# Performance work log

Measured on AMD Instinct MI355X. Metric: run time of the kernel, lower is better.

## Reference

```python
import jax, jax.numpy as jnp
import numpy as np

B, D, E, T, H = 16384, 1024, 8, 4, 512


def setup_inputs() -> dict:
    key = jax.random.key(0)
    ks = jax.random.split(key, 7)
    s_e = 1.0 / np.sqrt(D)
    s_t = 1.0 / np.sqrt(H)
    return {
        "x": jax.random.normal(ks[0], (B, D), dtype=jnp.float32),
        "We": jax.random.uniform(ks[1], (E, D, H), minval=-s_e, maxval=s_e, dtype=jnp.float32),
        "be": jax.random.uniform(ks[2], (E, H), minval=-s_e, maxval=s_e, dtype=jnp.float32),
        "Wg": jax.random.uniform(ks[3], (T, D, E), minval=-s_e, maxval=s_e, dtype=jnp.float32),
        "bg": jax.random.uniform(ks[4], (T, E), minval=-s_e, maxval=s_e, dtype=jnp.float32),
        "Wt": jax.random.uniform(ks[5], (T, H, 1), minval=-s_t, maxval=s_t, dtype=jnp.float32),
        "bt": jax.random.uniform(ks[6], (T, 1), minval=-s_t, maxval=s_t, dtype=jnp.float32),
    }


def reference(x, We, be, Wg, bg, Wt, bt):
    # Experts: [B, E, H] -- batched GEMM over all experts at once
    expert_out = jnp.einsum("bd,edh->beh", x, We) + be[None, :, :]
    # Gates per task: logits [B, T, E], softmax over experts
    gate_logits = jnp.einsum("bd,tde->bte", x, Wg) + bg[None, :, :]
    gate_w = jax.nn.softmax(gate_logits, axis=-1)
    # Weighted sum of expert outputs per task: [B, T, H]
    mixed = jnp.einsum("bte,beh->bth", gate_w, expert_out)
    # Task heads: [B, T, 1]
    task_out = jnp.einsum("bth,tho->bto", mixed, Wt) + bt[None, :, :]
    # Match original: list of T tensors [B, 1] -> stacked [T, B, 1]
    return jnp.transpose(task_out, (1, 0, 2))
```

## Files before the change

### kernel.cpp

```cpp
#include <hip/hip_runtime.h>
#include <math.h>


typedef float  f32x4  __attribute__((ext_vector_type(4)));
typedef short  bf16x8 __attribute__((ext_vector_type(8)));

#define WFRAG_OFF_BYTES 262272

__device__ __forceinline__ void cvt_pair(float f0, float f1, unsigned int& hi, unsigned int& lo) {
  unsigned int u0 = __float_as_uint(f0), u1 = __float_as_uint(f1);
  unsigned int r0 = u0 + 0x7FFFu + ((u0 >> 16) & 1u);
  unsigned int r1 = u1 + 0x7FFFu + ((u1 >> 16) & 1u);
  float h0 = __uint_as_float(r0 & 0xFFFF0000u);
  float h1 = __uint_as_float(r1 & 0xFFFF0000u);
  hi = (r0 >> 16) | (r1 & 0xFFFF0000u);
  float l0 = f0 - h0, l1 = f1 - h1;
  unsigned int s0 = __float_as_uint(l0), s1 = __float_as_uint(l1);
  unsigned int q0 = s0 + 0x7FFFu + ((s0 >> 16) & 1u);
  unsigned int q1 = s1 + 0x7FFFu + ((s1 >> 16) & 1u);
  lo = (q0 >> 16) | (q1 & 0xFFFF0000u);
}

__global__ __launch_bounds__(256) void mmoe_precompute(
    const float* __restrict__ We, const float* __restrict__ be,
    const float* __restrict__ Wg, const float* __restrict__ Wt,
    float* __restrict__ ws)
{
  float* Wcomb = ws;
  float* cbias = ws + 65536;
  const int tid = threadIdx.x, lane = tid & 63, w = tid >> 6;
  const int pairid = blockIdx.x * 4 + w;
  const int e = pairid >> 10, d = pairid & 1023;

  const float* werow = We + (size_t)pairid * 512;
  float a0 = 0.f, a1 = 0.f, a2 = 0.f, a3 = 0.f;
#pragma unroll
  for (int j = 0; j < 8; ++j) {
    int h = lane + j * 64;
    float wv = werow[h];
    a0 = fmaf(wv, Wt[h],        a0);
    a1 = fmaf(wv, Wt[512 + h],  a1);
    a2 = fmaf(wv, Wt[1024 + h], a2);
    a3 = fmaf(wv, Wt[1536 + h], a3);
  }
#pragma unroll
  for (int m = 1; m < 64; m <<= 1) {
    a0 += __shfl_xor(a0, m, 64); a1 += __shfl_xor(a1, m, 64);
    a2 += __shfl_xor(a2, m, 64); a3 += __shfl_xor(a3, m, 64);
  }
  if (lane == 0) {
    Wcomb[d * 64 + 32 + 0 * 8 + e] = a0;
    Wcomb[d * 64 + 32 + 1 * 8 + e] = a1;
    Wcomb[d * 64 + 32 + 2 * 8 + e] = a2;
    Wcomb[d * 64 + 32 + 3 * 8 + e] = a3;
  }
  if (e == 0 && lane < 32) {
    int t = lane >> 3, ee = lane & 7;
    Wcomb[d * 64 + t * 8 + ee] = Wg[t * 8192 + d * 8 + ee];
  }
  if (d == 0) {
    float b0 = 0.f, b1 = 0.f, b2 = 0.f, b3 = 0.f;
#pragma unroll
    for (int j = 0; j < 8; ++j) {
      int h = lane + j * 64;
      float bv = be[e * 512 + h];
      b0 = fmaf(bv, Wt[h],        b0);
      b1 = fmaf(bv, Wt[512 + h],  b1);
      b2 = fmaf(bv, Wt[1024 + h], b2);
      b3 = fmaf(bv, Wt[1536 + h], b3);
    }
#pragma unroll
    for (int m = 1; m < 64; m <<= 1) {
      b0 += __shfl_xor(b0, m, 64); b1 += __shfl_xor(b1, m, 64);
      b2 += __shfl_xor(b2, m, 64); b3 += __shfl_xor(b3, m, 64);
    }
    if (lane == 0) {
      cbias[0 * 8 + e] = b0; cbias[1 * 8 + e] = b1;
      cbias[2 * 8 + e] = b2; cbias[3 * 8 + e] = b3;
    }
  }
}

__global__ __launch_bounds__(256) void mmoe_swizzle(const float* __restrict__ Wc,
                                                    uint4* __restrict__ wf)
{
  const int idx = blockIdx.x * 256 + threadIdx.x;
  const int ks = idx >> 9;
  const int rem = idx & 511;
  const int vn = rem >> 6, l = rem & 63;
  const int v = vn >> 2, nf = vn & 3;
  const int n = nf * 16 + (l & 15);
  const int kbase = ks * 32 + (l >> 4) * 8;
  unsigned int pk[4];
#pragma unroll
  for (int p = 0; p < 4; ++p) {
    float f0 = Wc[(size_t)(kbase + 2 * p) * 64 + n];
    float f1 = Wc[(size_t)(kbase + 2 * p + 1) * 64 + n];
    unsigned int hi, lo;
    cvt_pair(f0, f1, hi, lo);
    pk[p] = v ? lo : hi;
  }
  uint4 val; val.x = pk[0]; val.y = pk[1]; val.z = pk[2]; val.w = pk[3];
  wf[idx] = val;
}

__global__ __launch_bounds__(64, 1) void mmoe_main(
    const float* __restrict__ x,
    const float* __restrict__ bgp,
    const float* __restrict__ btp,
    const float* __restrict__ ws,
    float* __restrict__ out)
{
  __shared__ float cmat[1024];
  const int l  = threadIdx.x;
  const int b0g = blockIdx.x * 16;
  const float* cbias = ws + 65536;
  const bf16x8* __restrict__ bptr =
      (const bf16x8*)((const unsigned char*)ws + WFRAG_OFF_BYTES);

  const float4* __restrict__ xptr =
      (const float4*)(x + (size_t)(b0g + (l & 15)) * 1024) + (l >> 4) * 2;

  float4 xbuf[4][2];
  bf16x8 breg[2][8];
  f32x4  acc[4];
#pragma unroll
  for (int nf = 0; nf < 4; ++nf) acc[nf] = (f32x4){0.f, 0.f, 0.f, 0.f};

#pragma unroll
  for (int p = 0; p < 4; ++p) { xbuf[p][0] = xptr[p * 8]; xbuf[p][1] = xptr[p * 8 + 1]; }
#pragma unroll
  for (int vn = 0; vn < 8; ++vn) breg[0][vn] = bptr[vn * 64 + l];
#pragma unroll
  for (int vn = 0; vn < 8; ++vn) breg[1][vn] = bptr[512 + vn * 64 + l];

  union UC { unsigned int u[4]; bf16x8 v; };

#define STEP(S)                                                                      \
  {                                                                                  \
    float4 xa = xbuf[(S) & 3][0], xb = xbuf[(S) & 3][1];                             \
    if ((S) + 4 < 32) {                                                              \
      xbuf[(S) & 3][0] = xptr[((S) + 4) * 8];                                        \
      xbuf[(S) & 3][1] = xptr[((S) + 4) * 8 + 1];                                    \
    }                                                                                \
    UC Ah, Al;                                                                       \
    cvt_pair(xa.x, xa.y, Ah.u[0], Al.u[0]);                                          \
    cvt_pair(xa.z, xa.w, Ah.u[1], Al.u[1]);                                          \
    cvt_pair(xb.x, xb.y, Ah.u[2], Al.u[2]);                                          \
    cvt_pair(xb.z, xb.w, Ah.u[3], Al.u[3]);                                          \
    acc[0] = __builtin_amdgcn_mfma_f32_16x16x32_bf16(Ah.v, breg[(S) & 1][0], acc[0], 0, 0, 0); \
    acc[1] = __builtin_amdgcn_mfma_f32_16x16x32_bf16(Ah.v, breg[(S) & 1][1], acc[1], 0, 0, 0); \
    acc[2] = __builtin_amdgcn_mfma_f32_16x16x32_bf16(Ah.v, breg[(S) & 1][2], acc[2], 0, 0, 0); \
    acc[3] = __builtin_amdgcn_mfma_f32_16x16x32_bf16(Ah.v, breg[(S) & 1][3], acc[3], 0, 0, 0); \
    acc[0] = __builtin_amdgcn_mfma_f32_16x16x32_bf16(Ah.v, breg[(S) & 1][4], acc[0], 0, 0, 0); \
    acc[1] = __builtin_amdgcn_mfma_f32_16x16x32_bf16(Ah.v, breg[(S) & 1][5], acc[1], 0, 0, 0); \
    acc[2] = __builtin_amdgcn_mfma_f32_16x16x32_bf16(Ah.v, breg[(S) & 1][6], acc[2], 0, 0, 0); \
    acc[3] = __builtin_amdgcn_mfma_f32_16x16x32_bf16(Ah.v, breg[(S) & 1][7], acc[3], 0, 0, 0); \
    acc[0] = __builtin_amdgcn_mfma_f32_16x16x32_bf16(Al.v, breg[(S) & 1][0], acc[0], 0, 0, 0); \
    acc[1] = __builtin_amdgcn_mfma_f32_16x16x32_bf16(Al.v, breg[(S) & 1][1], acc[1], 0, 0, 0); \
    acc[2] = __builtin_amdgcn_mfma_f32_16x16x32_bf16(Al.v, breg[(S) & 1][2], acc[2], 0, 0, 0); \
    acc[3] = __builtin_amdgcn_mfma_f32_16x16x32_bf16(Al.v, breg[(S) & 1][3], acc[3], 0, 0, 0); \
    if ((S) + 2 < 32) {                                                              \
      _Pragma("unroll")                                                              \
      for (int vn = 0; vn < 8; ++vn)                                                 \
        breg[(S) & 1][vn] = bptr[((S) + 2) * 512 + vn * 64 + l];                     \
    }                                                                                \
  }

  STEP(0)  STEP(1)  STEP(2)  STEP(3)  STEP(4)  STEP(5)  STEP(6)  STEP(7)
  STEP(8)  STEP(9)  STEP(10) STEP(11) STEP(12) STEP(13) STEP(14) STEP(15)
  STEP(16) STEP(17) STEP(18) STEP(19) STEP(20) STEP(21) STEP(22) STEP(23)
  STEP(24) STEP(25) STEP(26) STEP(27) STEP(28) STEP(29) STEP(30) STEP(31)
#undef STEP

#pragma unroll
  for (int nf = 0; nf < 4; ++nf)
#pragma unroll
    for (int r = 0; r < 4; ++r)
      cmat[((l >> 4) * 4 + r) * 64 + nf * 16 + (l & 15)] = acc[nf][r];
  __syncthreads();

  const int row = l >> 2, t = l & 3;
  const float4 ga = *(const float4*)&cmat[row * 64 + t * 8];
  const float4 gb = *(const float4*)&cmat[row * 64 + t * 8 + 4];
  const float4 sa = *(const float4*)&cmat[row * 64 + 32 + t * 8];
  const float4 sb = *(const float4*)&cmat[row * 64 + 32 + t * 8 + 4];
  float g[8] = {ga.x, ga.y, ga.z, ga.w, gb.x, gb.y, gb.z, gb.w};
  float s[8] = {sa.x, sa.y, sa.z, sa.w, sb.x, sb.y, sb.z, sb.w};
#pragma unroll
  for (int e = 0; e < 8; ++e) {
    g[e] += bgp[t * 8 + e];
    s[e] += cbias[t * 8 + e];
  }
  float m = g[0];
#pragma unroll
  for (int e = 1; e < 8; ++e) m = fmaxf(m, g[e]);
  float Z = 0.f, num = 0.f;
#pragma unroll
  for (int e = 0; e < 8; ++e) {
    float p = __expf(g[e] - m);
    Z += p;
    num = fmaf(p, s[e], num);
  }
  out[t * 16384 + b0g + row] = num / Z + btp[t];
}

extern "C" void kernel_launch(void* const* d_in, const int* in_sizes, int n_in,
                              void* d_out, int out_size, void* d_ws, size_t ws_size,
                              hipStream_t stream) {
  const float* x  = (const float*)d_in[0];
  const float* We = (const float*)d_in[1];
  const float* be = (const float*)d_in[2];
  const float* Wg = (const float*)d_in[3];
  const float* bg = (const float*)d_in[4];
  const float* Wt = (const float*)d_in[5];
  const float* bt = (const float*)d_in[6];
  float* out = (float*)d_out;
  float* ws  = (float*)d_ws;

  uint4* wf = (uint4*)((unsigned char*)d_ws + WFRAG_OFF_BYTES);

  hipLaunchKernelGGL(mmoe_precompute, dim3(2048), dim3(256), 0, stream, We, be, Wg, Wt, ws);
  hipLaunchKernelGGL(mmoe_swizzle,    dim3(64),   dim3(256), 0, stream, ws, wf);
  hipLaunchKernelGGL(mmoe_main,       dim3(1024), dim3(64),  0, stream, x, bg, bt, ws, out);
}
```

Measured before the change: 135.2 us.

## Process two 16-row tiles per wave to reuse weight fragments; use hardware bf16 convert

Each single-wave block now handles 32 batch rows as two 16-row MFMA tiles that share the same loaded weight fragments, halving weight-fragment traffic per row and the grid size to 512 blocks. The software round-to-nearest split of fp32 into bf16 hi/lo is replaced by the v_cvt_pk_bf16_f32 instruction, cutting VALU work per conversion. The epilogue loops twice per lane to cover the larger tile. This raises register pressure and halves the number of waves, which may reduce latency hiding on a large GPU.

```diff
diff --git a/kernel.cpp b/kernel.cpp
--- a/kernel.cpp
+++ b/kernel.cpp
@@ -21,6 +21,19 @@
   lo = (q0 >> 16) | (q1 & 0xFFFF0000u);
 }
 
+__device__ __forceinline__ unsigned int cvtpk_bf16(float a, float b) {
+  unsigned int r;
+  asm("v_cvt_pk_bf16_f32 %0, %1, %2" : "=v"(r) : "v"(a), "v"(b));
+  return r;
+}
+__device__ __forceinline__ void cvt_pair_fast(float f0, float f1, unsigned int& hi, unsigned int& lo) {
+  unsigned int h = cvtpk_bf16(f0, f1);
+  float h0 = __uint_as_float(h << 16);
+  float h1 = __uint_as_float(h & 0xFFFF0000u);
+  lo = cvtpk_bf16(f0 - h0, f1 - h1);
+  hi = h;
+}
+
 __global__ __launch_bounds__(256) void mmoe_precompute(
     const float* __restrict__ We, const float* __restrict__ be,
     const float* __restrict__ Wg, const float* __restrict__ Wt,
@@ -104,6 +117,65 @@
   wf[idx] = val;
 }
 
+union UC { unsigned int u[4]; bf16x8 v; };
+
+template <int S>
+__device__ __forceinline__ void mmoe_step(
+    const float4* __restrict__ xp0, const float4* __restrict__ xp1,
+    const bf16x8* __restrict__ bptr, int l,
+    float4 (&xbuf)[4][2][2], bf16x8 (&breg)[2][8], f32x4 (&acc)[2][4])
+{
+  constexpr int D = S & 3;
+  constexpr int P = S & 1;
+  float4 xa0 = xbuf[D][0][0], xa1 = xbuf[D][0][1];
+  float4 xb0 = xbuf[D][1][0], xb1 = xbuf[D][1][1];
+  if constexpr (S + 4 < 32) {
+    xbuf[D][0][0] = xp0[(S + 4) * 8];
+    xbuf[D][0][1] = xp0[(S + 4) * 8 + 1];
+    xbuf[D][1][0] = xp1[(S + 4) * 8];
+    xbuf[D][1][1] = xp1[(S + 4) * 8 + 1];
+  }
+  UC A0h, A0l, A1h, A1l;
+  cvt_pair_fast(xa0.x, xa0.y, A0h.u[0], A0l.u[0]);
+  cvt_pair_fast(xa0.z, xa0.w, A0h.u[1], A0l.u[1]);
+  cvt_pair_fast(xa1.x, xa1.y, A0h.u[2], A0l.u[2]);
+  cvt_pair_fast(xa1.z, xa1.w, A0h.u[3], A0l.u[3]);
+  cvt_pair_fast(xb0.x, xb0.y, A1h.u[0], A1l.u[0]);
+  cvt_pair_fast(xb0.z, xb0.w, A1h.u[1], A1l.u[1]);
+  cvt_pair_fast(xb1.x, xb1.y, A1h.u[2], A1l.u[2]);
+  cvt_pair_fast(xb1.z, xb1.w, A1h.u[3], A1l.u[3]);
+
+#pragma unroll
+  for (int j = 0; j < 4; ++j) {
+    acc[0][j] = __builtin_amdgcn_mfma_f32_16x16x32_bf16(A0h.v, breg[P][j], acc[0][j], 0, 0, 0);
+  }
+#pragma unroll
+  for (int j = 0; j < 4; ++j) {
+    acc[1][j] = __builtin_amdgcn_mfma_f32_16x16x32_bf16(A1h.v, breg[P][j], acc[1][j], 0, 0, 0);
+  }
+#pragma unroll
+  for (int j = 0; j < 4; ++j) {
+    acc[0][j] = __builtin_amdgcn_mfma_f32_16x16x32_bf16(A0h.v, breg[P][j + 4], acc[0][j], 0, 0, 0);
+  }
+#pragma unroll
+  for (int j = 0; j < 4; ++j) {
+    acc[1][j] = __builtin_amdgcn_mfma_f32_16x16x32_bf16(A1h.v, breg[P][j + 4], acc[1][j], 0, 0, 0);
+  }
+#pragma unroll
+  for (int j = 0; j < 4; ++j) {
+    acc[0][j] = __builtin_amdgcn_mfma_f32_16x16x32_bf16(A0l.v, breg[P][j], acc[0][j], 0, 0, 0);
+  }
+#pragma unroll
+  for (int j = 0; j < 4; ++j) {
+    acc[1][j] = __builtin_amdgcn_mfma_f32_16x16x32_bf16(A1l.v, breg[P][j], acc[1][j], 0, 0, 0);
+  }
+  if constexpr (S + 2 < 32) {
+#pragma unroll
+    for (int vn = 0; vn < 8; ++vn)
+      breg[P][vn] = bptr[(S + 2) * 512 + vn * 64 + l];
+  }
+}
+
 __global__ __launch_bounds__(64, 1) void mmoe_main(
     const float* __restrict__ x,
     const float* __restrict__ bgp,
@@ -111,98 +183,78 @@
     const float* __restrict__ ws,
     float* __restrict__ out)
 {
-  __shared__ float cmat[1024];
-  const int l  = threadIdx.x;
-  const int b0g = blockIdx.x * 16;
+  __shared__ float cmat[2048];
+  const int l   = threadIdx.x;
+  const int b0g = blockIdx.x * 32;
   const float* cbias = ws + 65536;
   const bf16x8* __restrict__ bptr =
       (const bf16x8*)((const unsigned char*)ws + WFRAG_OFF_BYTES);
 
-  const float4* __restrict__ xptr =
+  const float4* __restrict__ xp0 =
       (const float4*)(x + (size_t)(b0g + (l & 15)) * 1024) + (l >> 4) * 2;
-
-  float4 xbuf[4][2];
+  const float4* __restrict__ xp1 = xp0 + 16 * 256;
+
+  float4 xbuf[4][2][2];
   bf16x8 breg[2][8];
-  f32x4  acc[4];
-#pragma unroll
-  for (int nf = 0; nf < 4; ++nf) acc[nf] = (f32x4){0.f, 0.f, 0.f, 0.f};
-
-#pragma unroll
-  for (int p = 0; p < 4; ++p) { xbuf[p][0] = xptr[p * 8]; xbuf[p][1] = xptr[p * 8 + 1]; }
+  f32x4  acc[2][4];
+#pragma unroll
+  for (int f = 0; f < 2; ++f)
+#pragma unroll
+    for (int nf = 0; nf < 4; ++nf) acc[f][nf] = (f32x4){0.f, 0.f, 0.f, 0.f};
+
+#pragma unroll
+  for (int p = 0; p < 4; ++p) {
+    xbuf[p][0][0] = xp0[p * 8]; xbuf[p][0][1] = xp0[p * 8 + 1];
+    xbuf[p][1][0] = xp1[p * 8]; xbuf[p][1][1] = xp1[p * 8 + 1];
+  }
 #pragma unroll
   for (int vn = 0; vn < 8; ++vn) breg[0][vn] = bptr[vn * 64 + l];
 #pragma unroll
   for (int vn = 0; vn < 8; ++vn) breg[1][vn] = bptr[512 + vn * 64 + l];
 
-  union UC { unsigned int u[4]; bf16x8 v; };
-
-#define STEP(S)                                                                      \
-  {                                                                                  \
-    float4 xa = xbuf[(S) & 3][0], xb = xbuf[(S) & 3][1];                             \
-    if ((S) + 4 < 32) {                                                              \
-      xbuf[(S) & 3][0] = xptr[((S) + 4) * 8];                                        \
-      xbuf[(S) & 3][1] = xptr[((S) + 4) * 8 + 1];                                    \
-    }                                                                                \
-    UC Ah, Al;                                                                       \
-    cvt_pair(xa.x, xa.y, Ah.u[0], Al.u[0]);                                          \
-    cvt_pair(xa.z, xa.w, Ah.u[1], Al.u[1]);                                          \
-    cvt_pair(xb.x, xb.y, Ah.u[2], Al.u[2]);                                          \
-    cvt_pair(xb.z, xb.w, Ah.u[3], Al.u[3]);                                          \
-    acc[0] = __builtin_amdgcn_mfma_f32_16x16x32_bf16(Ah.v, breg[(S) & 1][0], acc[0], 0, 0, 0); \
-    acc[1] = __builtin_amdgcn_mfma_f32_16x16x32_bf16(Ah.v, breg[(S) & 1][1], acc[1], 0, 0, 0); \
-    acc[2] = __builtin_amdgcn_mfma_f32_16x16x32_bf16(Ah.v, breg[(S) & 1][2], acc[2], 0, 0, 0); \
-    acc[3] = __builtin_amdgcn_mfma_f32_16x16x32_bf16(Ah.v, breg[(S) & 1][3], acc[3], 0, 0, 0); \
-    acc[0] = __builtin_amdgcn_mfma_f32_16x16x32_bf16(Ah.v, breg[(S) & 1][4], acc[0], 0, 0, 0); \
-    acc[1] = __builtin_amdgcn_mfma_f32_16x16x32_bf16(Ah.v, breg[(S) & 1][5], acc[1], 0, 0, 0); \
-    acc[2] = __builtin_amdgcn_mfma_f32_16x16x32_bf16(Ah.v, breg[(S) & 1][6], acc[2], 0, 0, 0); \
-    acc[3] = __builtin_amdgcn_mfma_f32_16x16x32_bf16(Ah.v, breg[(S) & 1][7], acc[3], 0, 0, 0); \
-    acc[0] = __builtin_amdgcn_mfma_f32_16x16x32_bf16(Al.v, breg[(S) & 1][0], acc[0], 0, 0, 0); \
-    acc[1] = __builtin_amdgcn_mfma_f32_16x16x32_bf16(Al.v, breg[(S) & 1][1], acc[1], 0, 0, 0); \
-    acc[2] = __builtin_amdgcn_mfma_f32_16x16x32_bf16(Al.v, breg[(S) & 1][2], acc[2], 0, 0, 0); \
-    acc[3] = __builtin_amdgcn_mfma_f32_16x16x32_bf16(Al.v, breg[(S) & 1][3], acc[3], 0, 0, 0); \
-    if ((S) + 2 < 32) {                                                              \
-      _Pragma("unroll")                                                              \
-      for (int vn = 0; vn < 8; ++vn)                                                 \
-        breg[(S) & 1][vn] = bptr[((S) + 2) * 512 + vn * 64 + l];                     \
-    }                                                                                \
-  }
-
-  STEP(0)  STEP(1)  STEP(2)  STEP(3)  STEP(4)  STEP(5)  STEP(6)  STEP(7)
-  STEP(8)  STEP(9)  STEP(10) STEP(11) STEP(12) STEP(13) STEP(14) STEP(15)
-  STEP(16) STEP(17) STEP(18) STEP(19) STEP(20) STEP(21) STEP(22) STEP(23)
-  STEP(24) STEP(25) STEP(26) STEP(27) STEP(28) STEP(29) STEP(30) STEP(31)
-#undef STEP
-
-#pragma unroll
-  for (int nf = 0; nf < 4; ++nf)
-#pragma unroll
-    for (int r = 0; r < 4; ++r)
-      cmat[((l >> 4) * 4 + r) * 64 + nf * 16 + (l & 15)] = acc[nf][r];
+#define MSTEP(S) mmoe_step<S>(xp0, xp1, bptr, l, xbuf, breg, acc);
+  MSTEP(0)  MSTEP(1)  MSTEP(2)  MSTEP(3)  MSTEP(4)  MSTEP(5)  MSTEP(6)  MSTEP(7)
+  MSTEP(8)  MSTEP(9)  MSTEP(10) MSTEP(11) MSTEP(12) MSTEP(13) MSTEP(14) MSTEP(15)
+  MSTEP(16) MSTEP(17) MSTEP(18) MSTEP(19) MSTEP(20) MSTEP(21) MSTEP(22) MSTEP(23)
+  MSTEP(24) MSTEP(25) MSTEP(26) MSTEP(27) MSTEP(28) MSTEP(29) MSTEP(30) MSTEP(31)
+#undef MSTEP
+
+#pragma unroll
+  for (int f = 0; f < 2; ++f)
+#pragma unroll
+    for (int nf = 0; nf < 4; ++nf)
+#pragma unroll
+      for (int r = 0; r < 4; ++r)
+        cmat[(f * 16 + (l >> 4) * 4 + r) * 64 + nf * 16 + (l & 15)] = acc[f][nf][r];
   __syncthreads();
 
-  const int row = l >> 2, t = l & 3;
-  const float4 ga = *(const float4*)&cmat[row * 64 + t * 8];
-  const float4 gb = *(const float4*)&cmat[row * 64 + t * 8 + 4];
-  const float4 sa = *(const float4*)&cmat[row * 64 + 32 + t * 8];
-  const float4 sb = *(const float4*)&cmat[row * 64 + 32 + t * 8 + 4];
-  float g[8] = {ga.x, ga.y, ga.z, ga.w, gb.x, gb.y, gb.z, gb.w};
-  float s[8] = {sa.x, sa.y, sa.z, sa.w, sb.x, sb.y, sb.z, sb.w};
-#pragma unroll
-  for (int e = 0; e < 8; ++e) {
-    g[e] += bgp[t * 8 + e];
-    s[e] += cbias[t * 8 + e];
-  }
-  float m = g[0];
-#pragma unroll
-  for (int e = 1; e < 8; ++e) m = fmaxf(m, g[e]);
-  float Z = 0.f, num = 0.f;
-#pragma unroll
-  for (int e = 0; e < 8; ++e) {
-    float p = __expf(g[e] - m);
-    Z += p;
-    num = fmaf(p, s[e], num);
-  }
-  out[t * 16384 + b0g + row] = num / Z + btp[t];
+#pragma unroll
+  for (int p = 0; p < 2; ++p) {
+    const int idx = p * 64 + l;
+    const int row = idx >> 2, t = idx & 3;
+    const float4 ga = *(const float4*)&cmat[row * 64 + t * 8];
+    const float4 gb = *(const float4*)&cmat[row * 64 + t * 8 + 4];
+    const float4 sa = *(const float4*)&cmat[row * 64 + 32 + t * 8];
+    const float4 sb = *(const float4*)&cmat[row * 64 + 32 + t * 8 + 4];
+    float g[8] = {ga.x, ga.y, ga.z, ga.w, gb.x, gb.y, gb.z, gb.w};
+    float s[8] = {sa.x, sa.y, sa.z, sa.w, sb.x, sb.y, sb.z, sb.w};
+#pragma unroll
+    for (int e = 0; e < 8; ++e) {
+      g[e] += bgp[t * 8 + e];
+      s[e] += cbias[t * 8 + e];
+    }
+    float m = g[0];
+#pragma unroll
+    for (int e = 1; e < 8; ++e) m = fmaxf(m, g[e]);
+    float Z = 0.f, num = 0.f;
+#pragma unroll
+    for (int e = 0; e < 8; ++e) {
+      float p2 = __expf(g[e] - m);
+      Z += p2;
+      num = fmaf(p2, s[e], num);
+    }
+    out[t * 16384 + b0g + row] = num / Z + btp[t];
+  }
 }
 
 extern "C" void kernel_launch(void* const* d_in, const int* in_sizes, int n_in,
@@ -222,5 +274,5 @@
 
   hipLaunchKernelGGL(mmoe_precompute, dim3(2048), dim3(256), 0, stream, We, be, Wg, Wt, ws);
   hipLaunchKernelGGL(mmoe_swizzle,    dim3(64),   dim3(256), 0, stream, ws, wf);
-  hipLaunchKernelGGL(mmoe_main,       dim3(1024), dim3(64),  0, stream, x, bg, bt, ws, out);
-}
+  hipLaunchKernelGGL(mmoe_main,       dim3(512),  dim3(64),  0, stream, x, bg, bt, ws, out);
+}
```

Result: slower. 142.5 us (+5.4%).
